# Optimization experiments

Hardware: AMD Instinct MI355X
Metric: run time of the kernel (lower is better)

Reference implementation:

```python
import jax, jax.numpy as jnp
import numpy as np

N = 100000
E = 1600000
IN_C, HID_C, OUT_C = 128, 128, 64


def setup_inputs() -> dict:
    key = jax.random.key(0)
    ks = jax.random.split(key, 8)
    x = jax.random.normal(ks[0], (N, IN_C), dtype=jnp.float32)
    edge_index = jax.random.randint(ks[1], (2, E), 0, N, dtype=jnp.int64)
    # GCNConv weights (lin has no bias; bias added after aggregation)
    s1 = 1.0 / np.sqrt(IN_C)
    s2 = 1.0 / np.sqrt(HID_C)
    W1 = jax.random.uniform(ks[2], (IN_C, HID_C), jnp.float32, -s1, s1)
    b1 = jnp.zeros((HID_C,), jnp.float32)
    W2 = jax.random.uniform(ks[3], (HID_C, HID_C), jnp.float32, -s2, s2)
    b2 = jnp.zeros((HID_C,), jnp.float32)
    W3 = jax.random.uniform(ks[4], (HID_C, OUT_C), jnp.float32, -s2, s2)
    b3 = jnp.zeros((OUT_C,), jnp.float32)
    return {"x": x, "edge_index": edge_index, "W1": W1, "b1": b1,
            "W2": W2, "b2": b2, "W3": W3, "b3": b3}


def _prep_graph(edge_index):
    # add self-loops, compute symmetric normalization D^-1/2 A D^-1/2
    loop = jnp.arange(N, dtype=edge_index.dtype)
    src = jnp.concatenate([edge_index[0], loop])
    dst = jnp.concatenate([edge_index[1], loop])
    deg = jax.ops.segment_sum(jnp.ones_like(dst, dtype=jnp.float32), dst, num_segments=N)
    dinv = jnp.where(deg > 0, jax.lax.rsqrt(jnp.maximum(deg, 1e-12)), 0.0)
    norm = dinv[src] * dinv[dst]  # [E+N]
    return src, dst, norm


def _gcn_conv(x, W, b, src, dst, norm):
    h = x @ W                               # [N, C_out]
    msg = h[src] * norm[:, None]            # gather + scale, [E+N, C_out]
    out = jax.ops.segment_sum(msg, dst, num_segments=N)  # scatter-add
    return out + b


def reference(x, edge_index, W1, b1, W2, b2, W3, b3):
    src, dst, norm = _prep_graph(edge_index)
    h = jax.nn.relu(_gcn_conv(x, W1, b1, src, dst, norm))
    h = jax.nn.relu(_gcn_conv(h, W2, b2, src, dst, norm))
    return _gcn_conv(h, W3, b3, src, dst, norm)
```

## Files before the change

### kernel.cpp

```cpp
#include <hip/hip_runtime.h>
#include <hip/hip_bf16.h>
#include <hip/hip_fp16.h>

#define NN 100000
#define NE 1600000
constexpr int NN_PAD = 100032;
constexpr int NBUK = (NN + 255) / 256;
constexpr int CH   = 4096;
constexpr int EPT  = CH / 256;
constexpr int NCHK = (NE + CH - 1) / CH;
constexpr int LCNT = NBUK * NCHK;
constexpr int SCB  = (LCNT + 1023) / 1024;

typedef _Float16 f16x8 __attribute__((ext_vector_type(8)));
typedef float f32x4 __attribute__((ext_vector_type(4)));
typedef unsigned short u16x8 __attribute__((ext_vector_type(8)));

__device__ __forceinline__ float h2f(unsigned short h) {
    return __half2float(__ushort_as_half(h));
}
__device__ __forceinline__ unsigned short f2h(float f) {
    return __half_as_ushort(__float2half(f));
}

__global__ void k_detect_i64(const unsigned* __restrict__ ei, int* __restrict__ flag) {
    __shared__ int any_nz;
    if (threadIdx.x == 0) any_nz = 0;
    __syncthreads();
    int nz = 0;
    for (int i = threadIdx.x; i < 2048; i += 256)
        if (ei[2 * i + 1] != 0u) nz = 1;
    if (nz) atomicExch(&any_nz, 1);
    __syncthreads();
    if (threadIdx.x == 0) *flag = (any_nz == 0) ? 1 : 0;
}

__device__ __forceinline__ int edge_at(const void* ei, int is64, long long idx) {
    if (is64) return (int)((const long long*)ei)[idx];
    return ((const int*)ei)[idx];
}

__global__ __launch_bounds__(256) void k_count(const void* __restrict__ ei,
                                               const int* __restrict__ flag,
                                               int* __restrict__ counts) {
    __shared__ int cnt[NBUK];
    const int t = threadIdx.x, blk = blockIdx.x;
    for (int i = t; i < NBUK; i += 256) cnt[i] = 0;
    __syncthreads();
    const int is64 = *flag;
    const int e0 = blk * CH;
    const int elim = min(NE, e0 + CH);
#pragma unroll
    for (int j = 0; j < EPT; j++) {
        int e = e0 + j * 256 + t;
        if (e < elim) {
            int s = edge_at(ei, is64, e);
            int d = edge_at(ei, is64, (long long)NE + e);
            if ((unsigned)s < NN && (unsigned)d < NN) atomicAdd(&cnt[d >> 8], 1);
        }
    }
    __syncthreads();
    for (int i = t; i < NBUK; i += 256) counts[(size_t)i * NCHK + blk] = cnt[i];
}

__global__ void k_scan1v(int* __restrict__ data, int* __restrict__ bsum) {
    __shared__ int lds[256];
    int t = threadIdx.x, b = blockIdx.x;
    int base = b * 1024 + t * 4;
    int v0 = (base + 0 < LCNT) ? data[base + 0] : 0;
    int v1 = (base + 1 < LCNT) ? data[base + 1] : 0;
    int v2 = (base + 2 < LCNT) ? data[base + 2] : 0;
    int v3 = (base + 3 < LCNT) ? data[base + 3] : 0;
    lds[t] = v0 + v1 + v2 + v3;
    __syncthreads();
    for (int off = 1; off < 256; off <<= 1) {
        int x = (t >= off) ? lds[t - off] : 0;
        __syncthreads();
        lds[t] += x;
        __syncthreads();
    }
    int excl = (t > 0) ? lds[t - 1] : 0;
    if (t == 255) bsum[b] = lds[255];
    if (base + 0 < LCNT) data[base + 0] = excl;
    if (base + 1 < LCNT) data[base + 1] = excl + v0;
    if (base + 2 < LCNT) data[base + 2] = excl + v0 + v1;
    if (base + 3 < LCNT) data[base + 3] = excl + v0 + v1 + v2;
}

__global__ void k_scan2v(int* __restrict__ bsum) {
    __shared__ int lds[256];
    int t = threadIdx.x;
    int v = (t < SCB) ? bsum[t] : 0;
    lds[t] = v;
    __syncthreads();
    for (int off = 1; off < 256; off <<= 1) {
        int x = (t >= off) ? lds[t - off] : 0;
        __syncthreads();
        lds[t] += x;
        __syncthreads();
    }
    if (t < SCB) bsum[t] = lds[t] - v;
    if (t == SCB - 1) bsum[SCB] = lds[t];
}

__global__ void k_scan3v(int* __restrict__ data, const int* __restrict__ bsum) {
    int i = blockIdx.x * 256 + threadIdx.x;
    if (i < LCNT) data[i] += bsum[i >> 10];
    else if (i == LCNT) data[LCNT] = bsum[SCB];
}

__global__ __launch_bounds__(256) void k_scatter2(const void* __restrict__ ei,
                                                  const int* __restrict__ flag,
                                                  const int* __restrict__ scanned,
                                                  unsigned* __restrict__ staging) {
    __shared__ int cnt[512], excl[512], cur[512], gbase[512];
    __shared__ unsigned lbuf[CH];
    __shared__ unsigned short lbkt[CH];
    const int t = threadIdx.x, blk = blockIdx.x;
    cnt[t] = 0; cnt[t + 256] = 0;
    __syncthreads();
    const int is64 = *flag;
    const int e0 = blk * CH;
    const int elim = min(NE, e0 + CH);
    unsigned recs[EPT];
    int bkts[EPT];
#pragma unroll
    for (int j = 0; j < EPT; j++) {
        int e = e0 + j * 256 + t;
        int bk = -1; unsigned rc = 0;
        if (e < elim) {
            int s = edge_at(ei, is64, e);
            int d = edge_at(ei, is64, (long long)NE + e);
            if ((unsigned)s < NN && (unsigned)d < NN) {
                bk = d >> 8;
                rc = (unsigned)s | ((unsigned)(d & 255) << 17);
                atomicAdd(&cnt[bk], 1);
            }
        }
        recs[j] = rc; bkts[j] = bk;
    }
    __syncthreads();
    excl[t] = cnt[t]; excl[t + 256] = cnt[t + 256];
    __syncthreads();
    for (int off = 1; off < 512; off <<= 1) {
        int a0 = (t >= off) ? excl[t - off] : 0;
        int a1 = (t + 256 >= off) ? excl[t + 256 - off] : 0;
        __syncthreads();
        excl[t] += a0; excl[t + 256] += a1;
        __syncthreads();
    }
    int i0 = excl[t] - cnt[t], i1 = excl[t + 256] - cnt[t + 256];
    excl[t] = i0; excl[t + 256] = i1;
    cur[t] = i0; cur[t + 256] = i1;
    for (int b = t; b < NBUK; b += 256) gbase[b] = scanned[(size_t)b * NCHK + blk];
    __syncthreads();
#pragma unroll
    for (int j = 0; j < EPT; j++) {
        if (bkts[j] >= 0) {
            int pos = atomicAdd(&cur[bkts[j]], 1);
            lbuf[pos] = recs[j];
            lbkt[pos] = (unsigned short)bkts[j];
        }
    }
    __syncthreads();
    const int tot = excl[NBUK];
    for (int i = t; i < tot; i += 256) {
        int b = lbkt[i];
        staging[(size_t)gbase[b] + (i - excl[b])] = lbuf[i];
    }
}

__global__ __launch_bounds__(256) void k_phaseB2(const unsigned* __restrict__ staging,
                                                 const int* __restrict__ scanned,
                                                 float* __restrict__ dinv,
                                                 int* __restrict__ row_off,
                                                 int* __restrict__ csr) {
    __shared__ int cnt[256], excl[256], cur[256];
    __shared__ int buf[8192];
    const int t = threadIdx.x, b = blockIdx.x;
    const int node0 = b << 8;
    const int nlocal = min(256, NN - node0);
    const int seg_beg = scanned[(size_t)b * NCHK];
    const size_t nxt = (size_t)(b + 1) * NCHK;
    const int seg_end = scanned[nxt > (size_t)LCNT ? (size_t)LCNT : nxt];
    const int len = min(seg_end - seg_beg, 8192);
    cnt[t] = 0;
    __syncthreads();
    for (int i = t; i < len; i += 256) {
        unsigned r = staging[seg_beg + i];
        atomicAdd(&cnt[r >> 17], 1);
    }
    __syncthreads();
    excl[t] = cnt[t];
    __syncthreads();
    for (int off = 1; off < 256; off <<= 1) {
        int x = (t >= off) ? excl[t - off] : 0;
        __syncthreads();
        excl[t] += x;
        __syncthreads();
    }
    int ex = excl[t] - cnt[t];
    excl[t] = ex;
    cur[t] = ex;
    if (t < nlocal) {
        row_off[node0 + t] = seg_beg + ex;
        dinv[node0 + t] = rsqrtf((float)(cnt[t] + 1));
    }
    if (b == NBUK - 1 && t == 0) row_off[NN] = seg_end;
    __syncthreads();
    for (int i = t; i < len; i += 256) {
        unsigned r = staging[seg_beg + i];
        int pos = atomicAdd(&cur[r >> 17], 1);
        buf[pos] = (int)(r & 0x1FFFFu);
    }
    __syncthreads();
    for (int i = t; i < len; i += 256) csr[seg_beg + i] = buf[i];
}

template <int C>
__global__ void k_packW(const float* __restrict__ W, _Float16* __restrict__ P) {
    constexpr int NT = C / 16;
    int i = blockIdx.x * 256 + threadIdx.x;
    if (i >= 4 * NT * 512) return;
    int j = i & 7, lane = (i >> 3) & 63;
    int rest = i >> 9;
    int ct = rest % NT, kc = rest / NT;
    int k = kc * 32 + (lane >> 4) * 8 + j;
    int n = ct * 16 + (lane & 15);
    P[i] = (_Float16)W[k * C + n];
}

template <int C, bool F32SRC>
__global__ __launch_bounds__(256) void k_mgemm(const void* __restrict__ Xv,
                                               const _Float16* __restrict__ P,
                                               const float* __restrict__ dinv,
                                               unsigned short* __restrict__ H) {
    constexpr int NT = C / 16;
    const int tid = threadIdx.x, w = tid >> 6, lane = tid & 63;
    const int lr = lane & 15, lg = lane >> 4;
    const int row = blockIdx.x * 64 + w * 16 + lr;
    const int arow = F32SRC ? min(row, NN - 1) : row;
    f32x4 acc[NT];
#pragma unroll
    for (int t = 0; t < NT; t++) acc[t] = (f32x4){0.f, 0.f, 0.f, 0.f};
    const f16x8* __restrict__ Pp = (const f16x8*)P;
#pragma unroll
    for (int kc = 0; kc < 4; kc++) {
        f16x8 a;
        if (F32SRC) {
            const float* xp = (const float*)Xv + (size_t)arow * 128 + kc * 32 + lg * 8;
            float4 x0 = *(const float4*)xp;
            float4 x1 = *(const float4*)(xp + 4);
            a[0] = (_Float16)x0.x; a[1] = (_Float16)x0.y;
            a[2] = (_Float16)x0.z; a[3] = (_Float16)x0.w;
            a[4] = (_Float16)x1.x; a[5] = (_Float16)x1.y;
            a[6] = (_Float16)x1.z; a[7] = (_Float16)x1.w;
        } else {
            a = *(const f16x8*)((const _Float16*)Xv + (size_t)arow * 128 + kc * 32 + lg * 8);
        }
#pragma unroll
        for (int t = 0; t < NT; t++) {
            f16x8 b = Pp[(kc * NT + t) * 64 + lane];
            acc[t] = __builtin_amdgcn_mfma_f32_16x16x32_f16(a, b, acc[t], 0, 0, 0);
        }
    }
    const int orow0 = blockIdx.x * 64 + w * 16 + lg * 4;
    float dv[4];
#pragma unroll
    for (int r = 0; r < 4; r++) dv[r] = dinv[orow0 + r];
#pragma unroll
    for (int t = 0; t < NT; t++)
#pragma unroll
        for (int r = 0; r < 4; r++)
            H[(size_t)(orow0 + r) * C + t * 16 + lr] = f2h(acc[t][r] * dv[r]);
}

template <bool RELU>
__global__ __launch_bounds__(256) void k_agg128(const unsigned short* __restrict__ H,
                                                const int* __restrict__ row_off,
                                                const int* __restrict__ csr,
                                                const float* __restrict__ dinv,
                                                const float* __restrict__ bias,
                                                unsigned short* __restrict__ OUT) {
    const int tid = threadIdx.x;
    const int wid = tid >> 6, lane = tid & 63;
    const int q = lane >> 4, il = lane & 15;
    const int node = blockIdx.x * 16 + wid * 4 + q;
    const int beg = row_off[node];
    const int cnt = row_off[node + 1] - beg;
    int m1 = max(cnt, __shfl(cnt, lane ^ 16));
    const int tmax = max(m1, __shfl(m1, lane ^ 32));
    const u16x8* __restrict__ Hh = (const u16x8*)H;
    float acc[8] = {0.f, 0.f, 0.f, 0.f, 0.f, 0.f, 0.f, 0.f};
    for (int j0 = 0; j0 < tmax; j0 += 16) {
        int sidx = node;
        if (j0 + il < cnt) sidx = csr[beg + j0 + il];
        const int rem = min(16, tmax - j0);
        for (int u = 0; u < rem; u += 8) {
            u16x8 v[8]; float m[8];
#pragma unroll
            for (int k = 0; k < 8; k++) {
                int s = __shfl(sidx, q * 16 + u + k);
                v[k] = Hh[(size_t)s * 16 + il];
                m[k] = (j0 + u + k < cnt) ? 1.f : 0.f;
            }
#pragma unroll
            for (int k = 0; k < 8; k++)
#pragma unroll
                for (int e = 0; e < 8; e++)
                    acc[e] = fmaf(m[k], h2f(v[k][e]), acc[e]);
        }
    }
    u16x8 hv = Hh[(size_t)node * 16 + il];
#pragma unroll
    for (int e = 0; e < 8; e++) acc[e] += h2f(hv[e]);
    const float dv = dinv[node];
    float4 b0 = *(const float4*)&bias[il * 8];
    float4 b1 = *(const float4*)&bias[il * 8 + 4];
    float ob[8] = {b0.x, b0.y, b0.z, b0.w, b1.x, b1.y, b1.z, b1.w};
    u16x8 oh;
#pragma unroll
    for (int e = 0; e < 8; e++) {
        float o = fmaf(acc[e], dv, ob[e]);
        if (RELU) o = fmaxf(o, 0.f);
        oh[e] = f2h(o);
    }
    ((u16x8*)OUT)[(size_t)node * 16 + il] = oh;
}

__global__ __launch_bounds__(256) void k_agg64(const unsigned short* __restrict__ H,
                                               const int* __restrict__ row_off,
                                               const int* __restrict__ csr,
                                               const float* __restrict__ dinv,
                                               const float* __restrict__ bias,
                                               float* __restrict__ OUT) {
    const int tid = threadIdx.x;
    const int wid = tid >> 6, lane = tid & 63;
    const int q = lane >> 3, il = lane & 7;
    const int node = blockIdx.x * 32 + wid * 8 + q;
    const int beg = row_off[node];
    const int cnt = row_off[node + 1] - beg;
    int m1 = max(cnt, __shfl(cnt, lane ^ 8));
    m1 = max(m1, __shfl(m1, lane ^ 16));
    const int tmax = max(m1, __shfl(m1, lane ^ 32));
    const u16x8* __restrict__ Hh = (const u16x8*)H;
    float acc[8] = {0.f, 0.f, 0.f, 0.f, 0.f, 0.f, 0.f, 0.f};
    for (int j0 = 0; j0 < tmax; j0 += 8) {
        int sidx = node;
        if (j0 + il < cnt) sidx = csr[beg + j0 + il];
        u16x8 v[8]; float m[8];
#pragma unroll
        for (int k = 0; k < 8; k++) {
            int s = __shfl(sidx, q * 8 + k);
            v[k] = Hh[(size_t)s * 8 + il];
            m[k] = (j0 + k < cnt) ? 1.f : 0.f;
        }
#pragma unroll
        for (int k = 0; k < 8; k++)
#pragma unroll
            for (int e = 0; e < 8; e++)
                acc[e] = fmaf(m[k], h2f(v[k][e]), acc[e]);
    }
    u16x8 hv = Hh[(size_t)node * 8 + il];
#pragma unroll
    for (int e = 0; e < 8; e++) acc[e] += h2f(hv[e]);
    const float dv = dinv[node];
    float4 b0 = *(const float4*)&bias[il * 8];
    float4 b1 = *(const float4*)&bias[il * 8 + 4];
    float ob[8] = {b0.x, b0.y, b0.z, b0.w, b1.x, b1.y, b1.z, b1.w};
    float4 o0, o1;
    o0.x = fmaf(acc[0], dv, ob[0]); o0.y = fmaf(acc[1], dv, ob[1]);
    o0.z = fmaf(acc[2], dv, ob[2]); o0.w = fmaf(acc[3], dv, ob[3]);
    o1.x = fmaf(acc[4], dv, ob[4]); o1.y = fmaf(acc[5], dv, ob[5]);
    o1.z = fmaf(acc[6], dv, ob[6]); o1.w = fmaf(acc[7], dv, ob[7]);
    *(float4*)&OUT[(size_t)node * 64 + il * 8] = o0;
    *(float4*)&OUT[(size_t)node * 64 + il * 8 + 4] = o1;
}

extern "C" void kernel_launch(void* const* d_in, const int* in_sizes, int n_in,
                              void* d_out, int out_size, void* d_ws, size_t ws_size,
                              hipStream_t stream) {
    const float* x  = (const float*)d_in[0];
    const void*  ei = d_in[1];
    const float* W1 = (const float*)d_in[2];
    const float* b1 = (const float*)d_in[3];
    const float* W2 = (const float*)d_in[4];
    const float* b2 = (const float*)d_in[5];
    const float* W3 = (const float*)d_in[6];
    const float* b3 = (const float*)d_in[7];
    float* out = (float*)d_out;

    char* wsp = (char*)d_ws;
    size_t off = 0;
    auto alloc = [&](size_t bytes) -> void* {
        void* p = wsp + off;
        off += (bytes + 255) & ~(size_t)255;
        return p;
    };
    unsigned short* G = (unsigned short*)alloc((size_t)NN_PAD * 128 * 2);
    unsigned short* F = (unsigned short*)alloc((size_t)NN_PAD * 128 * 2);
    float* dinv    = (float*)alloc((size_t)NN_PAD * 4);
    int*   row_off = (int*)alloc(((size_t)NN + 1) * 4);
    int*   counts  = (int*)alloc(((size_t)LCNT + 1) * 4);
    int*   bsum    = (int*)alloc(((size_t)SCB + 1) * 4);
    int*   csr     = (int*)alloc((size_t)NE * 4);
    _Float16* P1   = (_Float16*)alloc((size_t)128 * 128 * 2);
    _Float16* P2   = (_Float16*)alloc((size_t)128 * 128 * 2);
    _Float16* P3   = (_Float16*)alloc((size_t)128 * 64 * 2);
    int*   flag    = (int*)alloc(256);
    if (off > ws_size) return;

    unsigned* staging = (unsigned*)G;

    k_detect_i64<<<1, 256, 0, stream>>>((const unsigned*)ei, flag);
    k_count<<<NCHK, 256, 0, stream>>>(ei, flag, counts);
    k_scan1v<<<SCB, 256, 0, stream>>>(counts, bsum);
    k_scan2v<<<1, 256, 0, stream>>>(bsum);
    k_scan3v<<<(LCNT + 1 + 255) / 256, 256, 0, stream>>>(counts, bsum);
    k_scatter2<<<NCHK, 256, 0, stream>>>(ei, flag, counts, staging);
    k_phaseB2<<<NBUK, 256, 0, stream>>>(staging, counts, dinv, row_off, csr);

    k_packW<128><<<64, 256, 0, stream>>>(W1, P1);
    k_packW<128><<<64, 256, 0, stream>>>(W2, P2);
    k_packW<64><<<32, 256, 0, stream>>>(W3, P3);

    constexpr int NBLK = NN_PAD / 64;
    k_mgemm<128, true><<<NBLK, 256, 0, stream>>>(x, P1, dinv, G);
    k_agg128<true><<<NN / 16, 256, 0, stream>>>(G, row_off, csr, dinv, b1, F);
    k_mgemm<128, false><<<NBLK, 256, 0, stream>>>(F, P2, dinv, G);
    k_agg128<true><<<NN / 16, 256, 0, stream>>>(G, row_off, csr, dinv, b2, F);
    k_mgemm<64, false><<<NBLK, 256, 0, stream>>>(F, P3, dinv, G);
    k_agg64<<<NN / 32, 256, 0, stream>>>(G, row_off, csr, dinv, b3, out);
}
```

Before: 247.9 us.

## Fuse aggregation with following GEMM via LDS tile; halve edge chunk size

The layer-1 and layer-2 aggregation kernels are merged with the next layer's MFMA GEMM. Each block aggregates 64 nodes into an XOR-swizzled LDS tile and multiplies it by the packed weights in place. This removes one full write and read of the N×128 fp16 intermediate per fused layer, plus two launches. It also halves the edge chunk size used in the CSR build and widens the scan to 8 elements per thread, and zeroes the padded dinv entries so padded rows are safe. The cost is fewer blocks for the gather phase (64 nodes per block in 4 serial iterations) and extra LDS use, which may lower gather occupancy and latency hiding.

```diff
diff --git a/kernel.cpp b/kernel.cpp
--- a/kernel.cpp
+++ b/kernel.cpp
@@ -6,11 +6,11 @@
 #define NE 1600000
 constexpr int NN_PAD = 100032;
 constexpr int NBUK = (NN + 255) / 256;
-constexpr int CH   = 4096;
+constexpr int CH   = 2048;
 constexpr int EPT  = CH / 256;
 constexpr int NCHK = (NE + CH - 1) / CH;
 constexpr int LCNT = NBUK * NCHK;
-constexpr int SCB  = (LCNT + 1023) / 1024;
+constexpr int SCB  = (LCNT + 2047) / 2048;
 
 typedef _Float16 f16x8 __attribute__((ext_vector_type(8)));
 typedef float f32x4 __attribute__((ext_vector_type(4)));
@@ -23,7 +23,8 @@
     return __half_as_ushort(__float2half(f));
 }
 
-__global__ void k_detect_i64(const unsigned* __restrict__ ei, int* __restrict__ flag) {
+__global__ void k_detect_i64(const unsigned* __restrict__ ei, int* __restrict__ flag,
+                             float* __restrict__ dinv) {
     __shared__ int any_nz;
     if (threadIdx.x == 0) any_nz = 0;
     __syncthreads();
@@ -31,6 +32,7 @@
     for (int i = threadIdx.x; i < 2048; i += 256)
         if (ei[2 * i + 1] != 0u) nz = 1;
     if (nz) atomicExch(&any_nz, 1);
+    if (threadIdx.x < NN_PAD - NN) dinv[NN + threadIdx.x] = 0.f;
     __syncthreads();
     if (threadIdx.x == 0) *flag = (any_nz == 0) ? 1 : 0;
 }
@@ -66,12 +68,14 @@
 __global__ void k_scan1v(int* __restrict__ data, int* __restrict__ bsum) {
     __shared__ int lds[256];
     int t = threadIdx.x, b = blockIdx.x;
-    int base = b * 1024 + t * 4;
-    int v0 = (base + 0 < LCNT) ? data[base + 0] : 0;
-    int v1 = (base + 1 < LCNT) ? data[base + 1] : 0;
-    int v2 = (base + 2 < LCNT) ? data[base + 2] : 0;
-    int v3 = (base + 3 < LCNT) ? data[base + 3] : 0;
-    lds[t] = v0 + v1 + v2 + v3;
+    int base = b * 2048 + t * 8;
+    int v[8], s = 0;
+#pragma unroll
+    for (int j = 0; j < 8; j++) {
+        v[j] = (base + j < LCNT) ? data[base + j] : 0;
+        s += v[j];
+    }
+    lds[t] = s;
     __syncthreads();
     for (int off = 1; off < 256; off <<= 1) {
         int x = (t >= off) ? lds[t - off] : 0;
@@ -79,12 +83,13 @@
         lds[t] += x;
         __syncthreads();
     }
-    int excl = (t > 0) ? lds[t - 1] : 0;
+    int run = (t > 0) ? lds[t - 1] : 0;
     if (t == 255) bsum[b] = lds[255];
-    if (base + 0 < LCNT) data[base + 0] = excl;
-    if (base + 1 < LCNT) data[base + 1] = excl + v0;
-    if (base + 2 < LCNT) data[base + 2] = excl + v0 + v1;
-    if (base + 3 < LCNT) data[base + 3] = excl + v0 + v1 + v2;
+#pragma unroll
+    for (int j = 0; j < 8; j++) {
+        if (base + j < LCNT) data[base + j] = run;
+        run += v[j];
+    }
 }
 
 __global__ void k_scan2v(int* __restrict__ bsum) {
@@ -105,7 +110,7 @@
 
 __global__ void k_scan3v(int* __restrict__ data, const int* __restrict__ bsum) {
     int i = blockIdx.x * 256 + threadIdx.x;
-    if (i < LCNT) data[i] += bsum[i >> 10];
+    if (i < LCNT) data[i] += bsum[i >> 11];
     else if (i == LCNT) data[LCNT] = bsum[SCB];
 }
 
@@ -230,34 +235,29 @@
     P[i] = (_Float16)W[k * C + n];
 }
 
-template <int C, bool F32SRC>
-__global__ __launch_bounds__(256) void k_mgemm(const void* __restrict__ Xv,
+__global__ __launch_bounds__(256) void k_mgemm(const float* __restrict__ X,
                                                const _Float16* __restrict__ P,
                                                const float* __restrict__ dinv,
                                                unsigned short* __restrict__ H) {
-    constexpr int NT = C / 16;
+    constexpr int NT = 8;
     const int tid = threadIdx.x, w = tid >> 6, lane = tid & 63;
     const int lr = lane & 15, lg = lane >> 4;
     const int row = blockIdx.x * 64 + w * 16 + lr;
-    const int arow = F32SRC ? min(row, NN - 1) : row;
+    const int arow = min(row, NN - 1);
     f32x4 acc[NT];
 #pragma unroll
     for (int t = 0; t < NT; t++) acc[t] = (f32x4){0.f, 0.f, 0.f, 0.f};
     const f16x8* __restrict__ Pp = (const f16x8*)P;
 #pragma unroll
     for (int kc = 0; kc < 4; kc++) {
+        const float* xp = X + (size_t)arow * 128 + kc * 32 + lg * 8;
+        float4 x0 = *(const float4*)xp;
+        float4 x1 = *(const float4*)(xp + 4);
         f16x8 a;
-        if (F32SRC) {
-            const float* xp = (const float*)Xv + (size_t)arow * 128 + kc * 32 + lg * 8;
-            float4 x0 = *(const float4*)xp;
-            float4 x1 = *(const float4*)(xp + 4);
-            a[0] = (_Float16)x0.x; a[1] = (_Float16)x0.y;
-            a[2] = (_Float16)x0.z; a[3] = (_Float16)x0.w;
-            a[4] = (_Float16)x1.x; a[5] = (_Float16)x1.y;
-            a[6] = (_Float16)x1.z; a[7] = (_Float16)x1.w;
-        } else {
-            a = *(const f16x8*)((const _Float16*)Xv + (size_t)arow * 128 + kc * 32 + lg * 8);
-        }
+        a[0] = (_Float16)x0.x; a[1] = (_Float16)x0.y;
+        a[2] = (_Float16)x0.z; a[3] = (_Float16)x0.w;
+        a[4] = (_Float16)x1.x; a[5] = (_Float16)x1.y;
+        a[6] = (_Float16)x1.z; a[7] = (_Float16)x1.w;
 #pragma unroll
         for (int t = 0; t < NT; t++) {
             f16x8 b = Pp[(kc * NT + t) * 64 + lane];
@@ -272,60 +272,95 @@
     for (int t = 0; t < NT; t++)
 #pragma unroll
         for (int r = 0; r < 4; r++)
-            H[(size_t)(orow0 + r) * C + t * 16 + lr] = f2h(acc[t][r] * dv[r]);
-}
-
-template <bool RELU>
-__global__ __launch_bounds__(256) void k_agg128(const unsigned short* __restrict__ H,
-                                                const int* __restrict__ row_off,
-                                                const int* __restrict__ csr,
-                                                const float* __restrict__ dinv,
-                                                const float* __restrict__ bias,
-                                                unsigned short* __restrict__ OUT) {
-    const int tid = threadIdx.x;
-    const int wid = tid >> 6, lane = tid & 63;
+            H[(size_t)(orow0 + r) * 128 + t * 16 + lr] = f2h(acc[t][r] * dv[r]);
+}
+
+template <int COUT>
+__global__ __launch_bounds__(256) void k_fuse(const unsigned short* __restrict__ H,
+                                              const int* __restrict__ row_off,
+                                              const int* __restrict__ csr,
+                                              const float* __restrict__ dinv,
+                                              const float* __restrict__ bias,
+                                              const _Float16* __restrict__ P,
+                                              unsigned short* __restrict__ G) {
+    __shared__ unsigned short T[64 * 128];
+    const int tid = threadIdx.x, w = tid >> 6, lane = tid & 63;
     const int q = lane >> 4, il = lane & 15;
-    const int node = blockIdx.x * 16 + wid * 4 + q;
-    const int beg = row_off[node];
-    const int cnt = row_off[node + 1] - beg;
-    int m1 = max(cnt, __shfl(cnt, lane ^ 16));
-    const int tmax = max(m1, __shfl(m1, lane ^ 32));
+    const int nodeBase = blockIdx.x * 64;
     const u16x8* __restrict__ Hh = (const u16x8*)H;
-    float acc[8] = {0.f, 0.f, 0.f, 0.f, 0.f, 0.f, 0.f, 0.f};
-    for (int j0 = 0; j0 < tmax; j0 += 16) {
-        int sidx = node;
-        if (j0 + il < cnt) sidx = csr[beg + j0 + il];
-        const int rem = min(16, tmax - j0);
-        for (int u = 0; u < rem; u += 8) {
-            u16x8 v[8]; float m[8];
-#pragma unroll
-            for (int k = 0; k < 8; k++) {
-                int s = __shfl(sidx, q * 16 + u + k);
-                v[k] = Hh[(size_t)s * 16 + il];
-                m[k] = (j0 + u + k < cnt) ? 1.f : 0.f;
-            }
-#pragma unroll
-            for (int k = 0; k < 8; k++)
-#pragma unroll
-                for (int e = 0; e < 8; e++)
-                    acc[e] = fmaf(m[k], h2f(v[k][e]), acc[e]);
-        }
-    }
-    u16x8 hv = Hh[(size_t)node * 16 + il];
-#pragma unroll
-    for (int e = 0; e < 8; e++) acc[e] += h2f(hv[e]);
-    const float dv = dinv[node];
+    u16x8* __restrict__ T8 = (u16x8*)T;
     float4 b0 = *(const float4*)&bias[il * 8];
     float4 b1 = *(const float4*)&bias[il * 8 + 4];
     float ob[8] = {b0.x, b0.y, b0.z, b0.w, b1.x, b1.y, b1.z, b1.w};
-    u16x8 oh;
-#pragma unroll
-    for (int e = 0; e < 8; e++) {
-        float o = fmaf(acc[e], dv, ob[e]);
-        if (RELU) o = fmaxf(o, 0.f);
-        oh[e] = f2h(o);
-    }
-    ((u16x8*)OUT)[(size_t)node * 16 + il] = oh;
+    for (int it = 0; it < 4; ++it) {
+        const int rloc = w * 16 + it * 4 + q;
+        const int node = nodeBase + rloc;
+        const int vnode = min(node, NN - 1);
+        const int beg = row_off[vnode];
+        int cnt = row_off[vnode + 1] - beg;
+        if (node >= NN) cnt = 0;
+        int m1 = max(cnt, __shfl(cnt, lane ^ 16));
+        const int tmax = max(m1, __shfl(m1, lane ^ 32));
+        float acc[8] = {0.f, 0.f, 0.f, 0.f, 0.f, 0.f, 0.f, 0.f};
+        for (int j0 = 0; j0 < tmax; j0 += 16) {
+            int sidx = vnode;
+            if (j0 + il < cnt) sidx = csr[beg + j0 + il];
+            const int rem = min(16, tmax - j0);
+            for (int u = 0; u < rem; u += 8) {
+                u16x8 v[8]; float m[8];
+#pragma unroll
+                for (int k = 0; k < 8; k++) {
+                    int s = __shfl(sidx, q * 16 + u + k);
+                    v[k] = Hh[(size_t)s * 16 + il];
+                    m[k] = (j0 + u + k < cnt) ? 1.f : 0.f;
+                }
+#pragma unroll
+                for (int k = 0; k < 8; k++)
+#pragma unroll
+                    for (int e = 0; e < 8; e++)
+                        acc[e] = fmaf(m[k], h2f(v[k][e]), acc[e]);
+            }
+        }
+        u16x8 hv = Hh[(size_t)vnode * 16 + il];
+#pragma unroll
+        for (int e = 0; e < 8; e++) acc[e] += h2f(hv[e]);
+        const float dv = (node < NN) ? dinv[node] : 0.f;
+        u16x8 oh;
+#pragma unroll
+        for (int e = 0; e < 8; e++) {
+            float o = fmaf(acc[e], dv, ob[e]);
+            o = fmaxf(o, 0.f);
+            oh[e] = f2h(o);
+        }
+        T8[rloc * 16 + (il ^ (rloc & 7))] = oh;
+    }
+    __syncthreads();
+    constexpr int NT = COUT / 16;
+    const int lr = lane & 15, lg = lane >> 4;
+    const int arow = w * 16 + lr;
+    f32x4 acc2[NT];
+#pragma unroll
+    for (int t = 0; t < NT; t++) acc2[t] = (f32x4){0.f, 0.f, 0.f, 0.f};
+    const f16x8* __restrict__ Pp = (const f16x8*)P;
+#pragma unroll
+    for (int kc = 0; kc < 4; kc++) {
+        int c8 = kc * 4 + lg;
+        f16x8 a = *(const f16x8*)&T8[arow * 16 + (c8 ^ (arow & 7))];
+#pragma unroll
+        for (int t = 0; t < NT; t++) {
+            f16x8 b = Pp[(kc * NT + t) * 64 + lane];
+            acc2[t] = __builtin_amdgcn_mfma_f32_16x16x32_f16(a, b, acc2[t], 0, 0, 0);
+        }
+    }
+    const int orow0 = nodeBase + w * 16 + lg * 4;
+    float dv2[4];
+#pragma unroll
+    for (int r = 0; r < 4; r++) dv2[r] = dinv[orow0 + r];
+#pragma unroll
+    for (int t = 0; t < NT; t++)
+#pragma unroll
+        for (int r = 0; r < 4; r++)
+            G[(size_t)(orow0 + r) * COUT + t * 16 + lr] = f2h(acc2[t][r] * dv2[r]);
 }
 
 __global__ __launch_bounds__(256) void k_agg64(const unsigned short* __restrict__ H,
@@ -412,7 +447,7 @@
 
     unsigned* staging = (unsigned*)G;
 
-    k_detect_i64<<<1, 256, 0, stream>>>((const unsigned*)ei, flag);
+    k_detect_i64<<<1, 256, 0, stream>>>((const unsigned*)ei, flag, dinv);
     k_count<<<NCHK, 256, 0, stream>>>(ei, flag, counts);
     k_scan1v<<<SCB, 256, 0, stream>>>(counts, bsum);
     k_scan2v<<<1, 256, 0, stream>>>(bsum);
@@ -425,10 +460,8 @@
     k_packW<64><<<32, 256, 0, stream>>>(W3, P3);
 
     constexpr int NBLK = NN_PAD / 64;
-    k_mgemm<128, true><<<NBLK, 256, 0, stream>>>(x, P1, dinv, G);
-    k_agg128<true><<<NN / 16, 256, 0, stream>>>(G, row_off, csr, dinv, b1, F);
-    k_mgemm<128, false><<<NBLK, 256, 0, stream>>>(F, P2, dinv, G);
-    k_agg128<true><<<NN / 16, 256, 0, stream>>>(G, row_off, csr, dinv, b2, F);
-    k_mgemm<64, false><<<NBLK, 256, 0, stream>>>(F, P3, dinv, G);
+    k_mgemm<<<NBLK, 256, 0, stream>>>(x, P1, dinv, G);
+    k_fuse<128><<<NBLK, 256, 0, stream>>>(G, row_off, csr, dinv, b1, P2, F);
+    k_fuse<64><<<NBLK, 256, 0, stream>>>(F, row_off, csr, dinv, b2, P3, G);
     k_agg64<<<NN / 32, 256, 0, stream>>>(G, row_off, csr, dinv, b3, out);
 }
```

Measured after the change: 245.4 us. No clear change (-1.0%).
